# Performance work log

Hardware: AMD Instinct MI355X
Metric: run time of the kernel (lower is better)

The kernel has to match this reference:

```python
import jax, jax.numpy as jnp
import numpy as np

N, E, F_IN, H, OUT = 50000, 1600000, 128, 128, 32
NEG_SLOPE = 0.2


def setup_inputs() -> dict:
    key = jax.random.key(0)
    ks = jax.random.split(key, 9)
    s = lambda fan: 1.0 / np.sqrt(fan)
    x = jax.random.normal(ks[0], (N, F_IN), jnp.float32)
    edge_index = jax.random.randint(ks[1], (2, E), 0, N, jnp.int64)
    Wl1 = jax.random.normal(ks[2], (F_IN, H), jnp.float32) * s(F_IN)
    Wr1 = jax.random.normal(ks[3], (F_IN, H), jnp.float32) * s(F_IN)
    att1 = jax.random.normal(ks[4], (H,), jnp.float32) * s(H)
    b1 = jnp.zeros((H,), jnp.float32)
    Wl2 = jax.random.normal(ks[5], (H, OUT), jnp.float32) * s(H)
    Wr2 = jax.random.normal(ks[6], (H, OUT), jnp.float32) * s(H)
    att2 = jax.random.normal(ks[7], (OUT,), jnp.float32) * s(OUT)
    b2 = jnp.zeros((OUT,), jnp.float32)
    return {"x": x, "edge_index": edge_index, "Wl1": Wl1, "Wr1": Wr1,
            "att1": att1, "b1": b1, "Wl2": Wl2, "Wr2": Wr2, "att2": att2, "b2": b2}


def gatv2_layer(x, Wl, Wr, att, bias, src, dst, num_nodes):
    # PyG GATv2Conv (heads=1, concat=True, add_self_loops handled by caller)
    xl = x @ Wl  # source-side transform  [N, C]
    xr = x @ Wr  # target-side transform  [N, C]
    e = jax.nn.leaky_relu(xl[src] + xr[dst], NEG_SLOPE)  # [E, C]
    logits = e @ att  # [E]
    # segment softmax over incoming edges of each destination node
    m = jax.ops.segment_max(logits, dst, num_segments=num_nodes)  # [N]
    expv = jnp.exp(logits - m[dst])
    denom = jax.ops.segment_sum(expv, dst, num_segments=num_nodes)  # [N]
    alpha = expv / (denom[dst] + 1e-16)  # [E]
    out = jax.ops.segment_sum(xl[src] * alpha[:, None], dst, num_segments=num_nodes)
    return out + bias


def reference(x, edge_index, Wl1, Wr1, att1, b1, Wl2, Wr2, att2, b2):
    # add self-loops (PyG add_self_loops=True default)
    loops = jnp.arange(N, dtype=edge_index.dtype)
    src = jnp.concatenate([edge_index[0], loops])
    dst = jnp.concatenate([edge_index[1], loops])
    h = gatv2_layer(x, Wl1, Wr1, att1, b1, src, dst, N)
    h = jax.nn.relu(h)
    h = gatv2_layer(h, Wl2, Wr2, att2, b2, src, dst, N)
    return jax.nn.relu(h)
```

## Files before the change

### kernel.cpp

```cpp
#include <hip/hip_runtime.h>
#include <hip/hip_bf16.h>

#define N_NODES 50000
#define E_EDGES 1600000
#define E_TOT   (E_EDGES + N_NODES)
#define NEG_SLOPE 0.2f

#define NB       196
#define S1_TILE  2048
#define NT       ((E_TOT + S1_TILE - 1) / S1_TILE)
#define S2_CAP   12288

typedef _Float16 h2 __attribute__((ext_vector_type(2)));
typedef _Float16 h4 __attribute__((ext_vector_type(4)));
typedef _Float16 h8 __attribute__((ext_vector_type(8)));

__device__ __forceinline__ float fdot2h(h2 a, h2 b, float c)
{
#if __has_builtin(__builtin_amdgcn_fdot2)
    return __builtin_amdgcn_fdot2(a, b, c, false);
#else
    return c + (float)a[0] * (float)b[0] + (float)a[1] * (float)b[1];
#endif
}

__device__ __forceinline__ h2 leaky_pk(h2 e)
{
    const h2 c06 = {(_Float16)0.6f, (_Float16)0.6f};
    const h2 c04 = {(_Float16)0.4f, (_Float16)0.4f};
    unsigned int u = __builtin_bit_cast(unsigned int, e) & 0x7FFF7FFFu;
    h2 ae = __builtin_bit_cast(h2, u);
    return c06 * e + c04 * ae;
}

__global__ __launch_bounds__(256) void transform1_gemm(
    const float* __restrict__ x,
    const float* __restrict__ Wl, const float* __restrict__ Wr,
    _Float16* __restrict__ xl, _Float16* __restrict__ xr)
{
    __shared__ float xs[32][128];
    __shared__ float ws[32][128];
    const int n0 = blockIdx.x * 128;
    const float* __restrict__ W = blockIdx.y ? Wr : Wl;
    _Float16* __restrict__ Y = blockIdx.y ? xr : xl;
    const int t = threadIdx.x;
    const int tc = t & 15;
    const int tn = t >> 4;

    float acc[2][4][2][4];
#pragma unroll
    for (int nh = 0; nh < 2; ++nh)
#pragma unroll
        for (int i = 0; i < 4; ++i)
#pragma unroll
            for (int ch = 0; ch < 2; ++ch)
#pragma unroll
                for (int j = 0; j < 4; ++j) acc[nh][i][ch][j] = 0.f;

    for (int k0 = 0; k0 < 128; k0 += 32) {
        {
            const int node = t >> 1;
            const int kh = (t & 1) * 16;
            const int gn = n0 + node;
#pragma unroll
            for (int q = 0; q < 4; ++q) {
                float4 v = make_float4(0.f, 0.f, 0.f, 0.f);
                if (gn < N_NODES)
                    v = *(const float4*)&x[(size_t)gn * 128 + k0 + kh + q * 4];
                xs[kh + q * 4 + 0][node] = v.x;
                xs[kh + q * 4 + 1][node] = v.y;
                xs[kh + q * 4 + 2][node] = v.z;
                xs[kh + q * 4 + 3][node] = v.w;
            }
        }
        {
            const int c = t & 127;
            const int kq = (t >> 7) * 16;
#pragma unroll
            for (int ii = 0; ii < 16; ++ii)
                ws[kq + ii][c] = W[(size_t)(k0 + kq + ii) * 128 + c];
        }
        __syncthreads();
#pragma unroll 4
        for (int kk = 0; kk < 32; ++kk) {
            float4 a0 = *(const float4*)&xs[kk][tn * 4];
            float4 a1 = *(const float4*)&xs[kk][64 + tn * 4];
            float4 b0 = *(const float4*)&ws[kk][tc * 4];
            float4 b1 = *(const float4*)&ws[kk][64 + tc * 4];
            const float an[2][4] = {{a0.x, a0.y, a0.z, a0.w}, {a1.x, a1.y, a1.z, a1.w}};
            const float bc[2][4] = {{b0.x, b0.y, b0.z, b0.w}, {b1.x, b1.y, b1.z, b1.w}};
#pragma unroll
            for (int nh = 0; nh < 2; ++nh)
#pragma unroll
                for (int i = 0; i < 4; ++i)
#pragma unroll
                    for (int ch = 0; ch < 2; ++ch)
#pragma unroll
                        for (int j = 0; j < 4; ++j)
                            acc[nh][i][ch][j] = fmaf(an[nh][i], bc[ch][j], acc[nh][i][ch][j]);
        }
        __syncthreads();
    }
#pragma unroll
    for (int nh = 0; nh < 2; ++nh)
#pragma unroll
        for (int i = 0; i < 4; ++i) {
            const int node = n0 + nh * 64 + tn * 4 + i;
            if (node < N_NODES) {
#pragma unroll
                for (int ch = 0; ch < 2; ++ch) {
                    h4 v;
                    v[0] = (_Float16)acc[nh][i][ch][0];
                    v[1] = (_Float16)acc[nh][i][ch][1];
                    v[2] = (_Float16)acc[nh][i][ch][2];
                    v[3] = (_Float16)acc[nh][i][ch][3];
                    *(h4*)&Y[(size_t)node * 128 + ch * 64 + tc * 4] = v;
                }
            }
        }
}

__global__ __launch_bounds__(256) void transform2_gemm(
    const _Float16* __restrict__ h,
    const float* __restrict__ Wl, const float* __restrict__ Wr,
    _Float16* __restrict__ hl, _Float16* __restrict__ hr)
{
    __shared__ float xs[32][128];
    __shared__ float ws[32][64];
    const int n0 = blockIdx.x * 128;
    const int t = threadIdx.x;
    const int tc = t & 15;
    const int tn = t >> 4;

    float acc[2][4][4];
#pragma unroll
    for (int nh = 0; nh < 2; ++nh)
#pragma unroll
        for (int i = 0; i < 4; ++i)
#pragma unroll
            for (int j = 0; j < 4; ++j) acc[nh][i][j] = 0.f;

    for (int k0 = 0; k0 < 128; k0 += 32) {
        {
            const int node = t >> 1;
            const int kh = (t & 1) * 16;
            const int gn = n0 + node;
            h8 v0 = {}, v1 = {};
            if (gn < N_NODES) {
                v0 = *(const h8*)&h[(size_t)gn * 128 + k0 + kh];
                v1 = *(const h8*)&h[(size_t)gn * 128 + k0 + kh + 8];
            }
#pragma unroll
            for (int q = 0; q < 8; ++q) {
                xs[kh + q][node] = (float)v0[q];
                xs[kh + 8 + q][node] = (float)v1[q];
            }
        }
        {
            const int c = t & 63;
            const int kq = (t >> 6) * 8;
            const float* __restrict__ Wm = (c < 32) ? Wl : Wr;
            const int wc = c & 31;
#pragma unroll
            for (int ii = 0; ii < 8; ++ii)
                ws[kq + ii][c] = Wm[(size_t)(k0 + kq + ii) * 32 + wc];
        }
        __syncthreads();
#pragma unroll 4
        for (int kk = 0; kk < 32; ++kk) {
            float4 a0 = *(const float4*)&xs[kk][tn * 4];
            float4 a1 = *(const float4*)&xs[kk][64 + tn * 4];
            float4 b = *(const float4*)&ws[kk][tc * 4];
            const float an[2][4] = {{a0.x, a0.y, a0.z, a0.w}, {a1.x, a1.y, a1.z, a1.w}};
            const float bc[4] = {b.x, b.y, b.z, b.w};
#pragma unroll
            for (int nh = 0; nh < 2; ++nh)
#pragma unroll
                for (int i = 0; i < 4; ++i)
#pragma unroll
                    for (int j = 0; j < 4; ++j)
                        acc[nh][i][j] = fmaf(an[nh][i], bc[j], acc[nh][i][j]);
        }
        __syncthreads();
    }
    _Float16* __restrict__ Y = (tc < 8) ? hl : hr;
    const int col = (tc < 8) ? tc * 4 : tc * 4 - 32;
#pragma unroll
    for (int nh = 0; nh < 2; ++nh)
#pragma unroll
        for (int i = 0; i < 4; ++i) {
            const int node = n0 + nh * 64 + tn * 4 + i;
            if (node < N_NODES) {
                h4 v;
                v[0] = (_Float16)acc[nh][i][0];
                v[1] = (_Float16)acc[nh][i][1];
                v[2] = (_Float16)acc[nh][i][2];
                v[3] = (_Float16)acc[nh][i][3];
                *(h4*)&Y[(size_t)node * 32 + col] = v;
            }
        }
}

__global__ __launch_bounds__(256) void tile_hist(
    const int* __restrict__ src, const int* __restrict__ dst,
    int* __restrict__ counts)
{
    __shared__ int hh[NB];
    const int t = threadIdx.x;
    const int base = blockIdx.x * S1_TILE;
    for (int i = t; i < NB; i += 256) hh[i] = 0;
    __syncthreads();
#pragma unroll
    for (int k = 0; k < S1_TILE / 256; ++k) {
        const int i = base + k * 256 + t;
        if (i < E_TOT) {
            const int d = (i < E_EDGES) ? dst[i] : (i - E_EDGES);
            atomicAdd(&hh[d >> 8], 1);
        }
    }
    __syncthreads();
    for (int b = t; b < NB; b += 256)
        counts[blockIdx.x * NB + b] = hh[b];
}

__global__ __launch_bounds__(1024) void row_scan(
    const int* __restrict__ counts, int* __restrict__ rstart,
    int* __restrict__ bcount)
{
    __shared__ int tmp[1024];
    const int b = blockIdx.x;
    const int t = threadIdx.x;
    const int v = (t < NT) ? counts[t * NB + b] : 0;
    tmp[t] = v;
    __syncthreads();
    for (int off = 1; off < 1024; off <<= 1) {
        int add = (t >= off) ? tmp[t - off] : 0;
        __syncthreads();
        tmp[t] += add;
        __syncthreads();
    }
    if (t < NT) rstart[b * NT + t] = tmp[t] - v;
    if (t == 1023) bcount[b] = tmp[1023];
}

__global__ __launch_bounds__(256) void bucket_base(
    const int* __restrict__ bcount, int* __restrict__ bbase)
{
    __shared__ int tmp[256];
    const int t = threadIdx.x;
    int v = (t < NB) ? bcount[t] : 0;
    tmp[t] = v;
    __syncthreads();
    for (int off = 1; off < 256; off <<= 1) {
        int add = (t >= off) ? tmp[t - off] : 0;
        __syncthreads();
        tmp[t] += add;
        __syncthreads();
    }
    if (t < NB) bbase[t] = tmp[t] - v;
    if (t == NB - 1) bbase[NB] = tmp[t];
}

__global__ __launch_bounds__(256) void tile_scatter(
    const int* __restrict__ src, const int* __restrict__ dst,
    const int* __restrict__ rstart, const int* __restrict__ bbase,
    unsigned int* __restrict__ bucket_data)
{
    __shared__ int hh[256];
    __shared__ int ls[256];
    __shared__ int cur[NB];
    __shared__ int rs[NB];
    __shared__ unsigned int srt[S1_TILE];
    const int t = threadIdx.x;
    const int tile = blockIdx.x;
    const int base = tile * S1_TILE;
    const int tcount = min(S1_TILE, E_TOT - base);

    hh[t] = 0;
    __syncthreads();

    int eb[S1_TILE / 256];
    unsigned int ee[S1_TILE / 256];
#pragma unroll
    for (int k = 0; k < S1_TILE / 256; ++k) {
        const int i = base + k * 256 + t;
        eb[k] = -1;
        if (i < E_TOT) {
            int s, d;
            if (i < E_EDGES) { s = src[i]; d = dst[i]; }
            else { s = i - E_EDGES; d = s; }
            const int b = d >> 8;
            eb[k] = b;
            ee[k] = ((unsigned)b << 24) | ((unsigned)(d & 255) << 16) | (unsigned)s;
            atomicAdd(&hh[b], 1);
        }
    }
    __syncthreads();
    {
        const int v = hh[t];
        ls[t] = v;
        __syncthreads();
        for (int off = 1; off < 256; off <<= 1) {
            int add = (t >= off) ? ls[t - off] : 0;
            __syncthreads();
            ls[t] += add;
            __syncthreads();
        }
        const int excl = ls[t] - v;
        if (t < NB) {
            cur[t] = excl;
            rs[t] = bbase[t] + rstart[t * NT + tile] - excl;
        }
    }
    __syncthreads();
#pragma unroll
    for (int k = 0; k < S1_TILE / 256; ++k) {
        if (eb[k] >= 0) {
            const int pos = atomicAdd(&cur[eb[k]], 1);
            srt[pos] = ee[k];
        }
    }
    __syncthreads();
    for (int i = t; i < tcount; i += 256) {
        const unsigned int e = srt[i];
        bucket_data[rs[e >> 24] + i] = e;
    }
}

__global__ __launch_bounds__(1024) void bucket_sort(
    const unsigned int* __restrict__ bucket_data,
    const int* __restrict__ bbase,
    int* __restrict__ offs, unsigned short* __restrict__ sorted_src)
{
    __shared__ int hist[256];
    __shared__ int cur[256];
    __shared__ int tmp[256];
    __shared__ unsigned short srt[S2_CAP];
    const int b = blockIdx.x;
    const int t = threadIdx.x;
    const int lo = bbase[b], hi = bbase[b + 1];
    const int c = hi - lo;
    if (t < 256) hist[t] = 0;
    __syncthreads();
    for (int i = t; i < c; i += 1024)
        atomicAdd(&hist[(bucket_data[lo + i] >> 16) & 255u], 1);
    __syncthreads();
    if (t < 256) tmp[t] = hist[t];
    __syncthreads();
    for (int off = 1; off < 256; off <<= 1) {
        int add = (t < 256 && t >= off) ? tmp[t - off] : 0;
        __syncthreads();
        if (t < 256) tmp[t] += add;
        __syncthreads();
    }
    if (t < 256) {
        const int excl = tmp[t] - hist[t];
        cur[t] = excl;
        const int node = b * 256 + t;
        if (node < N_NODES) offs[node] = lo + excl;
    }
    if (b == 0 && t == 0) offs[N_NODES] = E_TOT;
    __syncthreads();
    for (int i = t; i < c; i += 1024) {
        const unsigned int e = bucket_data[lo + i];
        const int pos = atomicAdd(&cur[(e >> 16) & 255u], 1);
        srt[pos] = (unsigned short)(e & 0xFFFFu);
    }
    __syncthreads();
    for (int i = t; i < c; i += 1024)
        sorted_src[lo + i] = srt[i];
}

template <int C, int LPG, typename OUT_T>
__global__ __launch_bounds__(256) void gat_edge_pass(
    const _Float16* __restrict__ xl, const _Float16* __restrict__ xr,
    const float* __restrict__ att, const float* __restrict__ bias,
    const int* __restrict__ offs, const unsigned short* __restrict__ ssrc,
    OUT_T* __restrict__ out)
{
    constexpr int GPB = 256 / LPG;
    static_assert(C == LPG * 8, "8 halves per lane");
    const int node = blockIdx.x * GPB + threadIdx.x / LPG;
    if (node >= N_NODES) return;
    const int lane = threadIdx.x % LPG;
    const int cb = lane * 8;

    h2 a2[4], r2[4];
    {
        const h8 rv = *(const h8*)(xr + (size_t)node * C + cb);
#pragma unroll
        for (int i = 0; i < 4; ++i) {
            h2 av = {(_Float16)att[cb + 2 * i], (_Float16)att[cb + 2 * i + 1]};
            a2[i] = av;
            h2 rr = {rv[2 * i], rv[2 * i + 1]};
            r2[i] = rr;
        }
    }
    float acc[8];
#pragma unroll
    for (int v = 0; v < 8; ++v) acc[v] = 0.f;
    float m = -3.0e38f, denom = 0.f;

    const int p1 = offs[node + 1];
    int p = offs[node];

    for (; p + 2 <= p1; p += 2) {
        const int s0 = ssrc[p];
        const int s1 = ssrc[p + 1];
        const h8 x0 = *(const h8*)(xl + (size_t)s0 * C + cb);
        const h8 x1 = *(const h8*)(xl + (size_t)s1 * C + cb);
        float dot0 = 0.f, dot1 = 0.f;
#pragma unroll
        for (int i = 0; i < 4; ++i) {
            h2 xa = {x0[2 * i], x0[2 * i + 1]};
            h2 xb = {x1[2 * i], x1[2 * i + 1]};
            h2 e0 = xa + r2[i];
            h2 e1 = xb + r2[i];
            dot0 = fdot2h(a2[i], leaky_pk(e0), dot0);
            dot1 = fdot2h(a2[i], leaky_pk(e1), dot1);
        }
#pragma unroll
        for (int off = LPG >> 1; off; off >>= 1) {
            dot0 += __shfl_xor(dot0, off);
            dot1 += __shfl_xor(dot1, off);
        }
        const float pm = fmaxf(dot0, dot1);
        if (__builtin_expect(pm > m + 8.f, 0)) {
            const float sc = __expf(m - pm);
            m = pm;
            denom *= sc;
#pragma unroll
            for (int v = 0; v < 8; ++v) acc[v] *= sc;
        }
        const float w0 = __expf(dot0 - m);
        const float w1 = __expf(dot1 - m);
        denom += w0 + w1;
        const h2 w2 = {(_Float16)w0, (_Float16)w1};
#pragma unroll
        for (int v = 0; v < 8; ++v) {
            h2 xp = {x0[v], x1[v]};
            acc[v] = fdot2h(w2, xp, acc[v]);
        }
    }
    if (p < p1) {
        const int s0 = ssrc[p];
        const h8 x0 = *(const h8*)(xl + (size_t)s0 * C + cb);
        float dot0 = 0.f;
#pragma unroll
        for (int i = 0; i < 4; ++i) {
            h2 xa = {x0[2 * i], x0[2 * i + 1]};
            h2 e0 = xa + r2[i];
            dot0 = fdot2h(a2[i], leaky_pk(e0), dot0);
        }
#pragma unroll
        for (int off = LPG >> 1; off; off >>= 1) dot0 += __shfl_xor(dot0, off);
        if (dot0 > m + 8.f) {
            const float sc = __expf(m - dot0);
            m = dot0;
            denom *= sc;
#pragma unroll
            for (int v = 0; v < 8; ++v) acc[v] *= sc;
        }
        const float w0 = __expf(dot0 - m);
        denom += w0;
        const h2 w2 = {(_Float16)w0, (_Float16)0.f};
#pragma unroll
        for (int v = 0; v < 8; ++v) {
            h2 xp = {x0[v], x0[v]};
            acc[v] = fdot2h(w2, xp, acc[v]);
        }
    }

    const float inv = 1.f / (denom + 1e-16f);
    if constexpr (sizeof(OUT_T) == 2) {
        h8 o;
#pragma unroll
        for (int v = 0; v < 8; ++v)
            o[v] = (_Float16)fmaxf(fmaf(acc[v], inv, bias[cb + v]), 0.f);
        *(h8*)&out[(size_t)node * C + cb] = o;
    } else {
        float4 o0, o1;
        o0.x = fmaxf(fmaf(acc[0], inv, bias[cb + 0]), 0.f);
        o0.y = fmaxf(fmaf(acc[1], inv, bias[cb + 1]), 0.f);
        o0.z = fmaxf(fmaf(acc[2], inv, bias[cb + 2]), 0.f);
        o0.w = fmaxf(fmaf(acc[3], inv, bias[cb + 3]), 0.f);
        o1.x = fmaxf(fmaf(acc[4], inv, bias[cb + 4]), 0.f);
        o1.y = fmaxf(fmaf(acc[5], inv, bias[cb + 5]), 0.f);
        o1.z = fmaxf(fmaf(acc[6], inv, bias[cb + 6]), 0.f);
        o1.w = fmaxf(fmaf(acc[7], inv, bias[cb + 7]), 0.f);
        *(float4*)&out[(size_t)node * C + cb] = o0;
        *(float4*)&out[(size_t)node * C + cb + 4] = o1;
    }
}

extern "C" void kernel_launch(void* const* d_in, const int* in_sizes, int n_in,
                              void* d_out, int out_size, void* d_ws, size_t ws_size,
                              hipStream_t stream)
{
    const float* x    = (const float*)d_in[0];
    const int*   ei   = (const int*)d_in[1];
    const float* Wl1  = (const float*)d_in[2];
    const float* Wr1  = (const float*)d_in[3];
    const float* att1 = (const float*)d_in[4];
    const float* b1   = (const float*)d_in[5];
    const float* Wl2  = (const float*)d_in[6];
    const float* Wr2  = (const float*)d_in[7];
    const float* att2 = (const float*)d_in[8];
    const float* b2   = (const float*)d_in[9];
    float* out = (float*)d_out;

    const int* e_src = ei;
    const int* e_dst = ei + E_EDGES;

    char* ws = (char*)d_ws;
    _Float16* xl = (_Float16*)(ws + 0);
    _Float16* xr = (_Float16*)(ws + 25600000);
    _Float16* h  = (_Float16*)(ws + 51200000);
    unsigned short* sorted_src = (unsigned short*)(ws + 76800000);
    int* offs   = (int*)(ws + 83400192);
    int* bbase  = (int*)(ws + 83600384);
    int* bcount = (int*)(ws + 83602432);
    unsigned int* bucket_data = (unsigned int*)(ws + 51200000);
    int* counts = (int*)(ws + 58000000);
    int* rstart = (int*)(ws + 58700000);
    _Float16* hl = xl;
    _Float16* hr = xr;

    transform1_gemm<<<dim3((N_NODES + 127) / 128, 2), 256, 0, stream>>>(
        x, Wl1, Wr1, xl, xr);

    tile_hist<<<NT, 256, 0, stream>>>(e_src, e_dst, counts);
    row_scan<<<NB, 1024, 0, stream>>>(counts, rstart, bcount);
    bucket_base<<<1, 256, 0, stream>>>(bcount, bbase);
    tile_scatter<<<NT, 256, 0, stream>>>(e_src, e_dst, rstart, bbase, bucket_data);
    bucket_sort<<<NB, 1024, 0, stream>>>(bucket_data, bbase, offs, sorted_src);

    gat_edge_pass<128, 16, _Float16><<<N_NODES * 16 / 256, 256, 0, stream>>>(
        xl, xr, att1, b1, offs, sorted_src, h);

    transform2_gemm<<<(N_NODES + 127) / 128, 256, 0, stream>>>(
        h, Wl2, Wr2, hl, hr);

    gat_edge_pass<32, 4, float><<<(N_NODES * 4 + 255) / 256, 256, 0, stream>>>(
        hl, hr, att2, b2, offs, sorted_src, out);
}
```

Measured before the change: 196.5 us.

## Use packed fp16 dot2 in GEMMs, fold leaky-relu into attention, unroll edges by four

Both transform GEMMs now stage their operands in shared memory as packed fp16 pairs and accumulate with fdot2, which halves shared-memory traffic and FMA instruction count but lowers input precision to fp16. The edge pass folds LeakyReLU into two scaled attention vectors (0.6*att·e + 0.4*att·|e|), removing the packed multiplies. It also processes four edges per iteration to expose more gather parallelism, at the cost of higher register pressure.

```diff
diff --git a/kernel.cpp b/kernel.cpp
--- a/kernel.cpp
+++ b/kernel.cpp
@@ -24,13 +24,10 @@
 #endif
 }
 
-__device__ __forceinline__ h2 leaky_pk(h2 e)
-{
-    const h2 c06 = {(_Float16)0.6f, (_Float16)0.6f};
-    const h2 c04 = {(_Float16)0.4f, (_Float16)0.4f};
+__device__ __forceinline__ h2 habs2(h2 e)
+{
     unsigned int u = __builtin_bit_cast(unsigned int, e) & 0x7FFF7FFFu;
-    h2 ae = __builtin_bit_cast(h2, u);
-    return c06 * e + c04 * ae;
+    return __builtin_bit_cast(h2, u);
 }
 
 __global__ __launch_bounds__(256) void transform1_gemm(
@@ -38,8 +35,8 @@
     const float* __restrict__ Wl, const float* __restrict__ Wr,
     _Float16* __restrict__ xl, _Float16* __restrict__ xr)
 {
-    __shared__ float xs[32][128];
-    __shared__ float ws[32][128];
+    __shared__ h2 xs2[16][128];
+    __shared__ h2 ws2[16][128];
     const int n0 = blockIdx.x * 128;
     const float* __restrict__ W = blockIdx.y ? Wr : Wl;
     _Float16* __restrict__ Y = blockIdx.y ? xr : xl;
@@ -67,37 +64,42 @@
                 float4 v = make_float4(0.f, 0.f, 0.f, 0.f);
                 if (gn < N_NODES)
                     v = *(const float4*)&x[(size_t)gn * 128 + k0 + kh + q * 4];
-                xs[kh + q * 4 + 0][node] = v.x;
-                xs[kh + q * 4 + 1][node] = v.y;
-                xs[kh + q * 4 + 2][node] = v.z;
-                xs[kh + q * 4 + 3][node] = v.w;
+                h2 p0 = {(_Float16)v.x, (_Float16)v.y};
+                h2 p1 = {(_Float16)v.z, (_Float16)v.w};
+                xs2[kh / 2 + q * 2 + 0][node] = p0;
+                xs2[kh / 2 + q * 2 + 1][node] = p1;
             }
         }
         {
             const int c = t & 127;
             const int kq = (t >> 7) * 16;
 #pragma unroll
-            for (int ii = 0; ii < 16; ++ii)
-                ws[kq + ii][c] = W[(size_t)(k0 + kq + ii) * 128 + c];
+            for (int ii = 0; ii < 8; ++ii) {
+                h2 pw = {(_Float16)W[(size_t)(k0 + kq + 2 * ii) * 128 + c],
+                         (_Float16)W[(size_t)(k0 + kq + 2 * ii + 1) * 128 + c]};
+                ws2[kq / 2 + ii][c] = pw;
+            }
         }
         __syncthreads();
 #pragma unroll 4
-        for (int kk = 0; kk < 32; ++kk) {
-            float4 a0 = *(const float4*)&xs[kk][tn * 4];
-            float4 a1 = *(const float4*)&xs[kk][64 + tn * 4];
-            float4 b0 = *(const float4*)&ws[kk][tc * 4];
-            float4 b1 = *(const float4*)&ws[kk][64 + tc * 4];
-            const float an[2][4] = {{a0.x, a0.y, a0.z, a0.w}, {a1.x, a1.y, a1.z, a1.w}};
-            const float bc[2][4] = {{b0.x, b0.y, b0.z, b0.w}, {b1.x, b1.y, b1.z, b1.w}};
-#pragma unroll
-            for (int nh = 0; nh < 2; ++nh)
-#pragma unroll
-                for (int i = 0; i < 4; ++i)
-#pragma unroll
-                    for (int ch = 0; ch < 2; ++ch)
-#pragma unroll
-                        for (int j = 0; j < 4; ++j)
-                            acc[nh][i][ch][j] = fmaf(an[nh][i], bc[ch][j], acc[nh][i][ch][j]);
+        for (int k2 = 0; k2 < 16; ++k2) {
+            h2 a0[4], a1[4], b0[4], b1[4];
+#pragma unroll
+            for (int j = 0; j < 4; ++j) {
+                a0[j] = xs2[k2][tn * 4 + j];
+                a1[j] = xs2[k2][64 + tn * 4 + j];
+                b0[j] = ws2[k2][tc * 4 + j];
+                b1[j] = ws2[k2][64 + tc * 4 + j];
+            }
+#pragma unroll
+            for (int i = 0; i < 4; ++i)
+#pragma unroll
+                for (int j = 0; j < 4; ++j) {
+                    acc[0][i][0][j] = fdot2h(a0[i], b0[j], acc[0][i][0][j]);
+                    acc[0][i][1][j] = fdot2h(a0[i], b1[j], acc[0][i][1][j]);
+                    acc[1][i][0][j] = fdot2h(a1[i], b0[j], acc[1][i][0][j]);
+                    acc[1][i][1][j] = fdot2h(a1[i], b1[j], acc[1][i][1][j]);
+                }
         }
         __syncthreads();
     }
@@ -125,8 +127,8 @@
     const float* __restrict__ Wl, const float* __restrict__ Wr,
     _Float16* __restrict__ hl, _Float16* __restrict__ hr)
 {
-    __shared__ float xs[32][128];
-    __shared__ float ws[32][64];
+    __shared__ h2 xs2[16][128];
+    __shared__ h2 ws2[16][64];
     const int n0 = blockIdx.x * 128;
     const int t = threadIdx.x;
     const int tc = t & 15;
@@ -151,9 +153,11 @@
                 v1 = *(const h8*)&h[(size_t)gn * 128 + k0 + kh + 8];
             }
 #pragma unroll
-            for (int q = 0; q < 8; ++q) {
-                xs[kh + q][node] = (float)v0[q];
-                xs[kh + 8 + q][node] = (float)v1[q];
+            for (int q = 0; q < 4; ++q) {
+                h2 p0 = {v0[2 * q], v0[2 * q + 1]};
+                h2 p1 = {v1[2 * q], v1[2 * q + 1]};
+                xs2[kh / 2 + q][node] = p0;
+                xs2[kh / 2 + 4 + q][node] = p1;
             }
         }
         {
@@ -162,24 +166,29 @@
             const float* __restrict__ Wm = (c < 32) ? Wl : Wr;
             const int wc = c & 31;
 #pragma unroll
-            for (int ii = 0; ii < 8; ++ii)
-                ws[kq + ii][c] = Wm[(size_t)(k0 + kq + ii) * 32 + wc];
+            for (int ii = 0; ii < 4; ++ii) {
+                h2 pw = {(_Float16)Wm[(size_t)(k0 + kq + 2 * ii) * 32 + wc],
+                         (_Float16)Wm[(size_t)(k0 + kq + 2 * ii + 1) * 32 + wc]};
+                ws2[kq / 2 + ii][c] = pw;
+            }
         }
         __syncthreads();
 #pragma unroll 4
-        for (int kk = 0; kk < 32; ++kk) {
-            float4 a0 = *(const float4*)&xs[kk][tn * 4];
-            float4 a1 = *(const float4*)&xs[kk][64 + tn * 4];
-            float4 b = *(const float4*)&ws[kk][tc * 4];
-            const float an[2][4] = {{a0.x, a0.y, a0.z, a0.w}, {a1.x, a1.y, a1.z, a1.w}};
-            const float bc[4] = {b.x, b.y, b.z, b.w};
-#pragma unroll
-            for (int nh = 0; nh < 2; ++nh)
-#pragma unroll
-                for (int i = 0; i < 4; ++i)
-#pragma unroll
-                    for (int j = 0; j < 4; ++j)
-                        acc[nh][i][j] = fmaf(an[nh][i], bc[j], acc[nh][i][j]);
+        for (int k2 = 0; k2 < 16; ++k2) {
+            h2 a0[4], a1[4], b[4];
+#pragma unroll
+            for (int j = 0; j < 4; ++j) {
+                a0[j] = xs2[k2][tn * 4 + j];
+                a1[j] = xs2[k2][64 + tn * 4 + j];
+                b[j] = ws2[k2][tc * 4 + j];
+            }
+#pragma unroll
+            for (int i = 0; i < 4; ++i)
+#pragma unroll
+                for (int j = 0; j < 4; ++j) {
+                    acc[0][i][j] = fdot2h(a0[i], b[j], acc[0][i][j]);
+                    acc[1][i][j] = fdot2h(a1[i], b[j], acc[1][i][j]);
+                }
         }
         __syncthreads();
     }
@@ -385,13 +394,15 @@
     const int lane = threadIdx.x % LPG;
     const int cb = lane * 8;
 
-    h2 a2[4], r2[4];
+    h2 a6[4], a4[4], r2[4];
     {
         const h8 rv = *(const h8*)(xr + (size_t)node * C + cb);
 #pragma unroll
         for (int i = 0; i < 4; ++i) {
-            h2 av = {(_Float16)att[cb + 2 * i], (_Float16)att[cb + 2 * i + 1]};
-            a2[i] = av;
+            const float av0 = att[cb + 2 * i], av1 = att[cb + 2 * i + 1];
+            h2 t6 = {(_Float16)(0.6f * av0), (_Float16)(0.6f * av1)};
+            h2 t4 = {(_Float16)(0.4f * av0), (_Float16)(0.4f * av1)};
+            a6[i] = t6; a4[i] = t4;
             h2 rr = {rv[2 * i], rv[2 * i + 1]};
             r2[i] = rr;
         }
@@ -404,27 +415,35 @@
     const int p1 = offs[node + 1];
     int p = offs[node];
 
-    for (; p + 2 <= p1; p += 2) {
-        const int s0 = ssrc[p];
-        const int s1 = ssrc[p + 1];
+    for (; p + 4 <= p1; p += 4) {
+        const int s0 = ssrc[p], s1 = ssrc[p + 1];
+        const int s2 = ssrc[p + 2], s3 = ssrc[p + 3];
         const h8 x0 = *(const h8*)(xl + (size_t)s0 * C + cb);
         const h8 x1 = *(const h8*)(xl + (size_t)s1 * C + cb);
-        float dot0 = 0.f, dot1 = 0.f;
+        const h8 x2 = *(const h8*)(xl + (size_t)s2 * C + cb);
+        const h8 x3 = *(const h8*)(xl + (size_t)s3 * C + cb);
+        float d0 = 0.f, d1 = 0.f, d2 = 0.f, d3 = 0.f;
 #pragma unroll
         for (int i = 0; i < 4; ++i) {
             h2 xa = {x0[2 * i], x0[2 * i + 1]};
             h2 xb = {x1[2 * i], x1[2 * i + 1]};
-            h2 e0 = xa + r2[i];
-            h2 e1 = xb + r2[i];
-            dot0 = fdot2h(a2[i], leaky_pk(e0), dot0);
-            dot1 = fdot2h(a2[i], leaky_pk(e1), dot1);
+            h2 xc = {x2[2 * i], x2[2 * i + 1]};
+            h2 xd = {x3[2 * i], x3[2 * i + 1]};
+            h2 e0 = xa + r2[i], e1 = xb + r2[i];
+            h2 e2 = xc + r2[i], e3 = xd + r2[i];
+            d0 = fdot2h(a6[i], e0, fdot2h(a4[i], habs2(e0), d0));
+            d1 = fdot2h(a6[i], e1, fdot2h(a4[i], habs2(e1), d1));
+            d2 = fdot2h(a6[i], e2, fdot2h(a4[i], habs2(e2), d2));
+            d3 = fdot2h(a6[i], e3, fdot2h(a4[i], habs2(e3), d3));
         }
 #pragma unroll
         for (int off = LPG >> 1; off; off >>= 1) {
-            dot0 += __shfl_xor(dot0, off);
-            dot1 += __shfl_xor(dot1, off);
-        }
-        const float pm = fmaxf(dot0, dot1);
+            d0 += __shfl_xor(d0, off);
+            d1 += __shfl_xor(d1, off);
+            d2 += __shfl_xor(d2, off);
+            d3 += __shfl_xor(d3, off);
+        }
+        const float pm = fmaxf(fmaxf(d0, d1), fmaxf(d2, d3));
         if (__builtin_expect(pm > m + 8.f, 0)) {
             const float sc = __expf(m - pm);
             m = pm;
@@ -432,42 +451,79 @@
 #pragma unroll
             for (int v = 0; v < 8; ++v) acc[v] *= sc;
         }
-        const float w0 = __expf(dot0 - m);
-        const float w1 = __expf(dot1 - m);
+        const float w0 = __expf(d0 - m), w1 = __expf(d1 - m);
+        const float w2 = __expf(d2 - m), w3 = __expf(d3 - m);
+        denom += (w0 + w1) + (w2 + w3);
+        const h2 wA = {(_Float16)w0, (_Float16)w1};
+        const h2 wB = {(_Float16)w2, (_Float16)w3};
+#pragma unroll
+        for (int v = 0; v < 8; ++v) {
+            h2 pA = {x0[v], x1[v]};
+            h2 pB = {x2[v], x3[v]};
+            acc[v] = fdot2h(wA, pA, fdot2h(wB, pB, acc[v]));
+        }
+    }
+    for (; p + 2 <= p1; p += 2) {
+        const int s0 = ssrc[p], s1 = ssrc[p + 1];
+        const h8 x0 = *(const h8*)(xl + (size_t)s0 * C + cb);
+        const h8 x1 = *(const h8*)(xl + (size_t)s1 * C + cb);
+        float d0 = 0.f, d1 = 0.f;
+#pragma unroll
+        for (int i = 0; i < 4; ++i) {
+            h2 xa = {x0[2 * i], x0[2 * i + 1]};
+            h2 xb = {x1[2 * i], x1[2 * i + 1]};
+            h2 e0 = xa + r2[i], e1 = xb + r2[i];
+            d0 = fdot2h(a6[i], e0, fdot2h(a4[i], habs2(e0), d0));
+            d1 = fdot2h(a6[i], e1, fdot2h(a4[i], habs2(e1), d1));
+        }
+#pragma unroll
+        for (int off = LPG >> 1; off; off >>= 1) {
+            d0 += __shfl_xor(d0, off);
+            d1 += __shfl_xor(d1, off);
+        }
+        const float pm = fmaxf(d0, d1);
+        if (__builtin_expect(pm > m + 8.f, 0)) {
+            const float sc = __expf(m - pm);
+            m = pm;
+            denom *= sc;
+#pragma unroll
+            for (int v = 0; v < 8; ++v) acc[v] *= sc;
+        }
+        const float w0 = __expf(d0 - m), w1 = __expf(d1 - m);
         denom += w0 + w1;
-        const h2 w2 = {(_Float16)w0, (_Float16)w1};
+        const h2 wA = {(_Float16)w0, (_Float16)w1};
 #pragma unroll
         for (int v = 0; v < 8; ++v) {
-            h2 xp = {x0[v], x1[v]};
-            acc[v] = fdot2h(w2, xp, acc[v]);
+            h2 pA = {x0[v], x1[v]};
+            acc[v] = fdot2h(wA, pA, acc[v]);
         }
     }
     if (p < p1) {
         const int s0 = ssrc[p];
         const h8 x0 = *(const h8*)(xl + (size_t)s0 * C + cb);
-        float dot0 = 0.f;
+        float d0 = 0.f;
 #pragma unroll
         for (int i = 0; i < 4; ++i) {
             h2 xa = {x0[2 * i], x0[2 * i + 1]};
             h2 e0 = xa + r2[i];
-            dot0 = fdot2h(a2[i], leaky_pk(e0), dot0);
-        }
-#pragma unroll
-        for (int off = LPG >> 1; off; off >>= 1) dot0 += __shfl_xor(dot0, off);
-        if (dot0 > m + 8.f) {
-            const float sc = __expf(m - dot0);
-            m = dot0;
+            d0 = fdot2h(a6[i], e0, fdot2h(a4[i], habs2(e0), d0));
+        }
+#pragma unroll
+        for (int off = LPG >> 1; off; off >>= 1) d0 += __shfl_xor(d0, off);
+        if (d0 > m + 8.f) {
+            const float sc = __expf(m - d0);
+            m = d0;
             denom *= sc;
 #pragma unroll
             for (int v = 0; v < 8; ++v) acc[v] *= sc;
         }
-        const float w0 = __expf(dot0 - m);
+        const float w0 = __expf(d0 - m);
         denom += w0;
-        const h2 w2 = {(_Float16)w0, (_Float16)0.f};
+        const h2 wA = {(_Float16)w0, (_Float16)0.f};
 #pragma unroll
         for (int v = 0; v < 8; ++v) {
-            h2 xp = {x0[v], x0[v]};
-            acc[v] = fdot2h(w2, xp, acc[v]);
+            h2 pA = {x0[v], x0[v]};
+            acc[v] = fdot2h(wA, pA, acc[v]);
         }
     }
 
```

New measurement: 171.4 us. -12.8%, faster.
